# Optimization experiments

Measured on AMD Instinct MI355X. Metric: run time of the kernel, lower is better.

Reference implementation:

```python
import jax, jax.numpy as jnp
import numpy as np

M, S = 1024, 256   # keyframe intervals x IMU steps per interval
K = M + 1          # keyframes

# ---- quaternion utils (xyzw convention, as pypose) ----

def quat_mul(q, r):
    qx, qy, qz, qw = q[..., 0], q[..., 1], q[..., 2], q[..., 3]
    rx, ry, rz, rw = r[..., 0], r[..., 1], r[..., 2], r[..., 3]
    return jnp.stack([
        qw * rx + qx * rw + qy * rz - qz * ry,
        qw * ry - qx * rz + qy * rw + qz * rx,
        qw * rz + qx * ry - qy * rx + qz * rw,
        qw * rw - qx * rx - qy * ry - qz * rz], axis=-1)

def quat_conj(q):
    return jnp.concatenate([-q[..., :3], q[..., 3:4]], axis=-1)

def quat_exp(phi):
    theta = jnp.linalg.norm(phi, axis=-1, keepdims=True)
    half = 0.5 * theta
    small = theta < 1e-6
    k = jnp.where(small, 0.5 - theta * theta / 48.0,
                  jnp.sin(half) / jnp.where(small, 1.0, theta))
    return jnp.concatenate([phi * k, jnp.cos(half)], axis=-1)

def quat_log(q):
    v, w = q[..., :3], q[..., 3:4]
    n = jnp.linalg.norm(v, axis=-1, keepdims=True)
    small = n < 1e-6
    theta = 2.0 * jnp.arctan2(n, w)
    scale = jnp.where(small, 2.0 / jnp.where(jnp.abs(w) < 1e-6, 1.0, w),
                      theta / jnp.where(small, 1.0, n))
    return v * scale

def quat_to_mat(q):
    x, y, z, w = q[..., 0], q[..., 1], q[..., 2], q[..., 3]
    r = jnp.stack([
        1 - 2 * (y * y + z * z), 2 * (x * y - z * w), 2 * (x * z + y * w),
        2 * (x * y + z * w), 1 - 2 * (x * x + z * z), 2 * (y * z - x * w),
        2 * (x * z - y * w), 2 * (y * z + x * w), 1 - 2 * (x * x + y * y)], axis=-1)
    return r.reshape(q.shape[:-1] + (3, 3))

def skew(v):
    x, y, z = v[..., 0], v[..., 1], v[..., 2]
    o = jnp.zeros_like(x)
    return jnp.stack([o, -z, y, z, o, -x, -y, x, o], axis=-1).reshape(v.shape[:-1] + (3, 3))

def build_F(R, a, w):
    # batched 15x15 continuous-time state-transition matrix (F_t in source)
    m = R.shape[0]
    I3 = jnp.eye(3, dtype=R.dtype)
    F = jnp.zeros((m, 15, 15), R.dtype)
    F = F.at[:, 0:3, 3:6].set(I3)
    F = F.at[:, 3:6, 6:9].set(-jnp.einsum('mij,mjk->mik', R, skew(a)))
    F = F.at[:, 3:6, 9:12].set(-R)
    F = F.at[:, 6:9, 6:9].set(-skew(w))
    F = F.at[:, 6:9, 12:15].set(-I3)
    return F

def imu_loss(acc, gyro, dt, bias_a, bias_w, g, init_rot, init_pos, init_vel,
             gt_rot, gt_pos, gt_vel, weights=(1.0, 1.0, 1.0)):
    m, s, _ = acc.shape
    dtype = acc.dtype
    I15 = jnp.eye(15, dtype=dtype)
    q0 = jnp.broadcast_to(jnp.array([0., 0., 0., 1.], dtype), (m, 4))
    carry0 = (q0, jnp.zeros((m, 3), dtype), jnp.zeros((m, 3), dtype),
              jnp.broadcast_to(I15, (m, 15, 15)))
    xs = (jnp.swapaxes(dt, 0, 1), jnp.swapaxes(acc, 0, 1), jnp.swapaxes(gyro, 0, 1),
          jnp.swapaxes(bias_a, 0, 1), jnp.swapaxes(bias_w, 0, 1))

    def step(carry, x):
        q, v, p, J = carry
        dti, a, w, ba, bw = x
        d = dti[:, None]
        a_w = jnp.einsum('mij,mj->mi', quat_to_mat(q), a)   # accel in segment-start frame
        p = p + v * d + 0.5 * a_w * d * d
        v = v + a_w * d
        q = quat_mul(q, quat_exp(w * d))
        R = quat_to_mat(q)                                  # post-update rotation (F_t usage)
        F = build_F(R, a - ba, w - bw)
        J = jnp.einsum('mij,mjk->mik', I15 + dti[:, None, None] * F, J)
        return (q, v, p, J), None

    (gamma_hat, beta_hat, alpha_hat, Jac), _ = jax.lax.scan(step, carry0, xs)

    ba0, bw0 = bias_a[:, 0, :], bias_w[:, 0, :]   # bias at keyframe start (kf index)
    alpha = (alpha_hat + jnp.einsum('mij,mj->mi', Jac[:, 0:3, 9:12], ba0)
             + jnp.einsum('mij,mj->mi', Jac[:, 0:3, 12:15], bw0))
    beta = (beta_hat + jnp.einsum('mij,mj->mi', Jac[:, 3:6, 9:12], ba0)
            + jnp.einsum('mij,mj->mi', Jac[:, 3:6, 12:15], bw0))
    dtheta = 0.5 * jnp.einsum('mij,mj->mi', Jac[:, 6:9, 12:15], bw0)
    gamma = quat_mul(gamma_hat, jnp.concatenate([dtheta, jnp.ones((m, 1), dtype)], axis=-1))

    def rot_step(r, dq):
        r2 = quat_mul(r, dq)
        return r2, r2
    _, rots = jax.lax.scan(rot_step, init_rot, gamma)
    rot = jnp.concatenate([init_rot[None], rots], axis=0)   # [K,4]

    kf_dt = jnp.sum(dt, axis=1)[:, None]                    # [M,1]
    R_wb = quat_to_mat(rot[:m])
    dvel = -g[None, :] * kf_dt + jnp.einsum('mij,mj->mi', R_wb, beta)
    vel = jnp.cumsum(jnp.concatenate([init_vel[None], dvel], axis=0), axis=0)
    dpos = (vel[:m] * kf_dt - 0.5 * g[None, :] * kf_dt * kf_dt
            + jnp.einsum('mij,mj->mi', R_wb, alpha))
    pos = jnp.cumsum(jnp.concatenate([init_pos[None], dpos], axis=0), axis=0)

    rot_err = quat_log(quat_mul(quat_conj(gt_rot), rot))
    return jnp.concatenate([weights[0] * rot_err,
                            weights[1] * (gt_pos - pos) ** 2,
                            weights[2] * (gt_vel - vel) ** 2], axis=0)  # [3K,3]

def setup_inputs() -> dict:
    key = jax.random.key(0)
    ks = jax.random.split(key, 11)
    f32 = jnp.float32
    def unit_quat(k, shape):
        q = jax.random.normal(k, shape + (4,), f32)
        return q / jnp.linalg.norm(q, axis=-1, keepdims=True)
    return {
        'acc': jax.random.normal(ks[0], (M, S, 3), f32),
        'gyro': 0.1 * jax.random.normal(ks[1], (M, S, 3), f32),
        'dt': 0.005 * jax.random.uniform(ks[2], (M, S), f32),  # ~200Hz IMU
        'bias_a': 0.01 * jax.random.normal(ks[3], (M, S, 3), f32),
        'bias_w': 0.01 * jax.random.normal(ks[4], (M, S, 3), f32),
        'g': jnp.array([0.0, 0.0, 9.81007], f32),
        'init_rot': unit_quat(ks[5], ()),
        'init_pos': jax.random.normal(ks[6], (3,), f32),
        'init_vel': jax.random.normal(ks[7], (3,), f32),
        'gt_rot': unit_quat(ks[8], (K,)),
        'gt_pos': jax.random.normal(ks[9], (K, 3), f32),
        'gt_vel': jax.random.normal(ks[10], (K, 3), f32),
    }

def reference(acc, gyro, dt, bias_a, bias_w, g, init_rot, init_pos, init_vel,
              gt_rot, gt_pos, gt_vel):
    return imu_loss(acc, gyro, dt, bias_a, bias_w, g, init_rot, init_pos, init_vel,
                    gt_rot, gt_pos, gt_vel)
```

## Files before the change

### kernel.cpp

```cpp
#include <hip/hip_runtime.h>
#include <math.h>

#define NM 1024
#define NS 256
#define NK 1025
#define CS 4
#define NC 64

struct Q4 { float x, y, z, w; };

__device__ __forceinline__ Q4 qmul(const Q4 a, const Q4 b) {
    Q4 o;
    o.x = a.w*b.x + a.x*b.w + a.y*b.z - a.z*b.y;
    o.y = a.w*b.y - a.x*b.z + a.y*b.w + a.z*b.x;
    o.z = a.w*b.z + a.x*b.y - a.y*b.x + a.z*b.w;
    o.w = a.w*b.w - a.x*b.x - a.y*b.y - a.z*b.z;
    return o;
}

__device__ __forceinline__ void q2m(const Q4 q, float* R) {
    float x = q.x, y = q.y, z = q.z, w = q.w;
    R[0] = 1.f - 2.f*(y*y + z*z); R[1] = 2.f*(x*y - z*w);       R[2] = 2.f*(x*z + y*w);
    R[3] = 2.f*(x*y + z*w);       R[4] = 1.f - 2.f*(x*x + z*z); R[5] = 2.f*(y*z - x*w);
    R[6] = 2.f*(x*z - y*w);       R[7] = 2.f*(y*z + x*w);       R[8] = 1.f - 2.f*(x*x + y*y);
}

__device__ __forceinline__ void m3mul(float* o, const float* X, const float* Y) {
    #pragma unroll
    for (int r = 0; r < 3; ++r)
        #pragma unroll
        for (int c = 0; c < 3; ++c)
            o[r*3+c] = X[r*3+0]*Y[c] + X[r*3+1]*Y[3+c] + X[r*3+2]*Y[6+c];
}

__device__ __forceinline__ void m3v(float* o, const float* X, const float* v) {
    o[0] = X[0]*v[0] + X[1]*v[1] + X[2]*v[2];
    o[1] = X[3]*v[0] + X[4]*v[1] + X[5]*v[2];
    o[2] = X[6]*v[0] + X[7]*v[1] + X[8]*v[2];
}

__device__ __forceinline__ void skmul(float* o, float x, float y, float z, const float* M) {
    #pragma unroll
    for (int c = 0; c < 3; ++c) {
        float m0 = M[c], m1 = M[3+c], m2 = M[6+c];
        o[c]   = -z*m1 + y*m2;
        o[3+c] =  z*m0 - x*m2;
        o[6+c] = -y*m0 + x*m1;
    }
}

__device__ __forceinline__ void crossv(float* o, float x, float y, float z, const float* v) {
    o[0] = -z*v[1] + y*v[2];
    o[1] =  z*v[0] - x*v[2];
    o[2] = -y*v[0] + x*v[1];
}

__device__ __forceinline__ void ld12(float* dst, const float4* src) {
    float4 t0 = src[0], t1 = src[1], t2 = src[2];
    dst[0]=t0.x; dst[1]=t0.y; dst[2] =t0.z; dst[3] =t0.w;
    dst[4]=t1.x; dst[5]=t1.y; dst[6] =t1.z; dst[7] =t1.w;
    dst[8]=t2.x; dst[9]=t2.y; dst[10]=t2.z; dst[11]=t2.w;
}

__global__ __launch_bounds__(256, 2) void imu_phase1(
    const float* __restrict__ acc, const float* __restrict__ gyro,
    const float* __restrict__ dt, const float* __restrict__ bias_a,
    const float* __restrict__ bias_w, float* __restrict__ ws)
{
    const int lane = threadIdx.x & 63;
    const int m    = blockIdx.x * 4 + (threadIdx.x >> 6);
    const int c    = lane;

    float av[12], gv[12], bav[12], bwv[12], dtv[4];
    ld12(av,  (const float4*)(acc    + (size_t)m*NS*3) + c*3);
    ld12(gv,  (const float4*)(gyro   + (size_t)m*NS*3) + c*3);
    ld12(bav, (const float4*)(bias_a + (size_t)m*NS*3) + c*3);
    ld12(bwv, (const float4*)(bias_w + (size_t)m*NS*3) + c*3);
    {
        float4 t = ((const float4*)(dt + (size_t)m*NS))[c];
        dtv[0]=t.x; dtv[1]=t.y; dtv[2]=t.z; dtv[3]=t.w;
    }

    float ba0[3], bw0[3];
    ba0[0] = __shfl(bav[0], 0, 64); ba0[1] = __shfl(bav[1], 0, 64); ba0[2] = __shfl(bav[2], 0, 64);
    bw0[0] = __shfl(bwv[0], 0, 64); bw0[1] = __shfl(bwv[1], 0, 64); bw0[2] = __shfl(bwv[2], 0, 64);

    Q4 fq = {0.f, 0.f, 0.f, 1.f};
    float G[9] = {1.f,0.f,0.f, 0.f,1.f,0.f, 0.f,0.f,1.f};
    float T = 0.f;
    float u[3] = {0.f}, z[3] = {0.f};
    float A[9]  = {1.f,0.f,0.f, 0.f,1.f,0.f, 0.f,0.f,1.f};
    float Bmv[3] = {0.f};
    float M1v[3] = {0.f}, N[9] = {0.f}, nnv[3] = {0.f};
    float K1v[3] = {0.f}, K2a[9] = {0.f}, k2bv[3] = {0.f};

    #pragma unroll
    for (int j = 0; j < CS; ++j) {
        float d  = dtv[j];
        float ax = av[j*3+0], ay = av[j*3+1], az = av[j*3+2];
        float gx = gv[j*3+0], gy = gv[j*3+1], gz = gv[j*3+2];
        float abx = ax - bav[j*3+0], aby = ay - bav[j*3+1], abz = az - bav[j*3+2];
        float wbx = gx - bwv[j*3+0], wby = gy - bwv[j*3+1], wbz = gz - bwv[j*3+2];

        #pragma unroll
        for (int i = 0; i < 3; ++i) { K1v[i] += d*M1v[i]; k2bv[i] += d*nnv[i]; }
        #pragma unroll
        for (int i = 0; i < 9; ++i) K2a[i] += d*N[i];

        float ga0 = G[0]*ax + G[1]*ay + G[2]*az;
        float ga1 = G[3]*ax + G[4]*ay + G[5]*az;
        float ga2 = G[6]*ax + G[7]*ay + G[8]*az;
        float hd2 = 0.5f*d*d;
        z[0] += d*u[0] + hd2*ga0;
        z[1] += d*u[1] + hd2*ga1;
        z[2] += d*u[2] + hd2*ga2;
        u[0] += d*ga0; u[1] += d*ga1; u[2] += d*ga2;
        T += d;

        float phx = gx*d, phy = gy*d, phz = gz*d;
        float th2 = phx*phx + phy*phy + phz*phz;
        float k  = 0.5f - th2*(1.0f/48.0f);
        float ew = 1.0f - th2*0.125f;
        Q4 e = {phx*k, phy*k, phz*k, ew};
        fq = qmul(fq, e);
        q2m(fq, G);

        {
            float gb[3]; m3v(gb, G, ba0);
            M1v[0] += d*gb[0]; M1v[1] += d*gb[1]; M1v[2] += d*gb[2];
        }
        {
            float SA[9], GX[9];
            skmul(SA, abx, aby, abz, A);
            m3mul(GX, G, SA);
            #pragma unroll
            for (int i = 0; i < 9; ++i) N[i] += d*GX[i];
        }
        {
            float cb[3], gc[3];
            crossv(cb, abx, aby, abz, Bmv);
            m3v(gc, G, cb);
            nnv[0] += d*gc[0]; nnv[1] += d*gc[1]; nnv[2] += d*gc[2];
        }
        {
            float WA[9];
            skmul(WA, wbx, wby, wbz, A);
            #pragma unroll
            for (int i = 0; i < 9; ++i) A[i] -= d*WA[i];
        }
        {
            float cw[3];
            crossv(cw, wbx, wby, wbz, Bmv);
            Bmv[0] -= d*(cw[0] + bw0[0]);
            Bmv[1] -= d*(cw[1] + bw0[1]);
            Bmv[2] -= d*(cw[2] + bw0[2]);
        }
    }

    Q4 qi = fq;
    #pragma unroll
    for (int off = 1; off < 64; off <<= 1) {
        Q4 y;
        y.x = __shfl_up(qi.x, off, 64);
        y.y = __shfl_up(qi.y, off, 64);
        y.z = __shfl_up(qi.z, off, 64);
        y.w = __shfl_up(qi.w, off, 64);
        if (lane >= off) qi = qmul(y, qi);
    }
    Q4 qf;
    qf.x = __shfl(qi.x, 63, 64);
    qf.y = __shfl(qi.y, 63, 64);
    qf.z = __shfl(qi.z, 63, 64);
    qf.w = __shfl(qi.w, 63, 64);
    Q4 qp;
    qp.x = __shfl_up(qi.x, 1, 64);
    qp.y = __shfl_up(qi.y, 1, 64);
    qp.z = __shfl_up(qi.z, 1, 64);
    qp.w = __shfl_up(qi.w, 1, 64);
    if (lane == 0) { qp.x = 0.f; qp.y = 0.f; qp.z = 0.f; qp.w = 1.f; }
    float R[9]; q2m(qp, R);

    float bvec[3] = {Bmv[0], Bmv[1], Bmv[2]};
    #pragma unroll
    for (int off = 1; off < 64; off <<= 1) {
        float yA[9], yb[3];
        #pragma unroll
        for (int i = 0; i < 9; ++i) yA[i] = __shfl_up(A[i], off, 64);
        yb[0] = __shfl_up(bvec[0], off, 64);
        yb[1] = __shfl_up(bvec[1], off, 64);
        yb[2] = __shfl_up(bvec[2], off, 64);
        if (lane >= off) {
            float nA[9], nb[3];
            m3mul(nA, A, yA);
            m3v(nb, A, yb);
            #pragma unroll
            for (int i = 0; i < 9; ++i) A[i] = nA[i];
            bvec[0] = nb[0] + bvec[0];
            bvec[1] = nb[1] + bvec[1];
            bvec[2] = nb[2] + bvec[2];
        }
    }
    float Q2fv[3];
    Q2fv[0] = __shfl(bvec[0], 63, 64);
    Q2fv[1] = __shfl(bvec[1], 63, 64);
    Q2fv[2] = __shfl(bvec[2], 63, 64);
    float qv[3];
    qv[0] = __shfl_up(bvec[0], 1, 64);
    qv[1] = __shfl_up(bvec[1], 1, 64);
    qv[2] = __shfl_up(bvec[2], 1, 64);
    if (lane == 0) { qv[0] = 0.f; qv[1] = 0.f; qv[2] = 0.f; }

    float S = T;
    #pragma unroll
    for (int off = 1; off < 64; off <<= 1) {
        float y = __shfl_down(S, off, 64);
        if (lane + off < 64) S += y;
    }
    float Tsuf = S - T;

    float nq[3], kq[3];
    m3v(nq, N, qv);
    m3v(kq, K2a, qv);
    float t1[3] = { u[0] - M1v[0] - nq[0] - nnv[0],
                    u[1] - M1v[1] - nq[1] - nnv[1],
                    u[2] - M1v[2] - nq[2] - nnv[2] };
    float t2[3] = { z[0] - K1v[0] - kq[0] - k2bv[0],
                    z[1] - K1v[1] - kq[1] - k2bv[1],
                    z[2] - K1v[2] - kq[2] - k2bv[2] };
    float bc[3], ac[3];
    m3v(bc, R, t1);
    m3v(ac, R, t2);
    ac[0] += Tsuf*bc[0]; ac[1] += Tsuf*bc[1]; ac[2] += Tsuf*bc[2];

    #pragma unroll
    for (int off = 1; off < 64; off <<= 1) {
        #pragma unroll
        for (int i = 0; i < 3; ++i) {
            bc[i] += __shfl_xor(bc[i], off, 64);
            ac[i] += __shfl_xor(ac[i], off, 64);
        }
    }

    if (lane != 0) return;

    float dthx = 0.5f*Q2fv[0], dthy = 0.5f*Q2fv[1], dthz = 0.5f*Q2fv[2];
    Q4 dq = {dthx, dthy, dthz, 1.0f};
    Q4 gamma = qmul(qf, dq);

    float* g_gamma = ws;
    float* g_beta  = ws + 4*NM;
    float* g_alpha = ws + 7*NM;
    float* g_kf    = ws + 10*NM;
    g_gamma[m*4+0] = gamma.x; g_gamma[m*4+1] = gamma.y;
    g_gamma[m*4+2] = gamma.z; g_gamma[m*4+3] = gamma.w;
    g_beta[m*3+0] = bc[0];  g_beta[m*3+1] = bc[1];  g_beta[m*3+2] = bc[2];
    g_alpha[m*3+0] = ac[0]; g_alpha[m*3+1] = ac[1]; g_alpha[m*3+2] = ac[2];
    g_kf[m] = S;
}

__global__ __launch_bounds__(1024) void imu_phase2(
    const float* __restrict__ ws, const float* __restrict__ g,
    const float* __restrict__ init_rot, const float* __restrict__ init_pos,
    const float* __restrict__ init_vel, const float* __restrict__ gt_rot,
    const float* __restrict__ gt_pos, const float* __restrict__ gt_vel,
    float* __restrict__ out)
{
    __shared__ float4 srot[NK];
    __shared__ float  svel[NK][3];
    __shared__ float  spos[NK][3];
    __shared__ float4 qtot[16];
    __shared__ float  vtot[16][3];
    __shared__ float  ptot[16][3];

    const int tid  = threadIdx.x;
    const int lane = tid & 63;
    const int w    = tid >> 6;

    const float* g_gamma = ws;
    const float* g_beta  = ws + 4*NM;
    const float* g_alpha = ws + 7*NM;
    const float* g_kf    = ws + 10*NM;

    Q4 qinit = {init_rot[0], init_rot[1], init_rot[2], init_rot[3]};

    Q4 q = {g_gamma[tid*4+0], g_gamma[tid*4+1], g_gamma[tid*4+2], g_gamma[tid*4+3]};
    #pragma unroll
    for (int off = 1; off < 64; off <<= 1) {
        Q4 y;
        y.x = __shfl_up(q.x, off, 64);
        y.y = __shfl_up(q.y, off, 64);
        y.z = __shfl_up(q.z, off, 64);
        y.w = __shfl_up(q.w, off, 64);
        if (lane >= off) q = qmul(y, q);
    }
    if (lane == 63) qtot[w] = make_float4(q.x, q.y, q.z, q.w);
    __syncthreads();
    {
        Q4 pre = {0.f, 0.f, 0.f, 1.f};
        for (int j = 0; j < w; ++j) {
            float4 tq = qtot[j];
            pre = qmul(pre, Q4{tq.x, tq.y, tq.z, tq.w});
        }
        q = qmul(pre, q);
    }
    Q4 rot = qmul(qinit, q);
    srot[tid+1] = make_float4(rot.x, rot.y, rot.z, rot.w);
    if (tid == 0) srot[0] = make_float4(qinit.x, qinit.y, qinit.z, qinit.w);
    __syncthreads();

    const float gx = g[0], gy = g[1], gz = g[2];
    const float iv0 = init_vel[0], iv1 = init_vel[1], iv2 = init_vel[2];
    const float ip0 = init_pos[0], ip1 = init_pos[1], ip2 = init_pos[2];

    float4 r4 = srot[tid];
    Q4 rq = {r4.x, r4.y, r4.z, r4.w};
    float Rw[9]; q2m(rq, Rw);
    float kf = g_kf[tid];
    float bx = g_beta[tid*3+0], by = g_beta[tid*3+1], bz = g_beta[tid*3+2];
    float axm = g_alpha[tid*3+0], aym = g_alpha[tid*3+1], azm = g_alpha[tid*3+2];

    float dv0 = -gx*kf + Rw[0]*bx + Rw[1]*by + Rw[2]*bz;
    float dv1 = -gy*kf + Rw[3]*bx + Rw[4]*by + Rw[5]*bz;
    float dv2 = -gz*kf + Rw[6]*bx + Rw[7]*by + Rw[8]*bz;
    float s0 = dv0, s1 = dv1, s2 = dv2;
    #pragma unroll
    for (int off = 1; off < 64; off <<= 1) {
        float y0 = __shfl_up(s0, off, 64);
        float y1 = __shfl_up(s1, off, 64);
        float y2 = __shfl_up(s2, off, 64);
        if (lane >= off) { s0 += y0; s1 += y1; s2 += y2; }
    }
    if (lane == 63) { vtot[w][0] = s0; vtot[w][1] = s1; vtot[w][2] = s2; }
    __syncthreads();
    {
        float p0 = 0.f, p1 = 0.f, p2 = 0.f;
        for (int j = 0; j < w; ++j) { p0 += vtot[j][0]; p1 += vtot[j][1]; p2 += vtot[j][2]; }
        s0 += p0; s1 += p1; s2 += p2;
    }
    svel[tid+1][0] = iv0 + s0; svel[tid+1][1] = iv1 + s1; svel[tid+1][2] = iv2 + s2;
    if (tid == 0) { svel[0][0] = iv0; svel[0][1] = iv1; svel[0][2] = iv2; }

    float vm0 = iv0 + s0 - dv0, vm1 = iv1 + s1 - dv1, vm2 = iv2 + s2 - dv2;

    float dp0 = vm0*kf - 0.5f*gx*kf*kf + Rw[0]*axm + Rw[1]*aym + Rw[2]*azm;
    float dp1 = vm1*kf - 0.5f*gy*kf*kf + Rw[3]*axm + Rw[4]*aym + Rw[5]*azm;
    float dp2 = vm2*kf - 0.5f*gz*kf*kf + Rw[6]*axm + Rw[7]*aym + Rw[8]*azm;
    float t0 = dp0, t1 = dp1, t2 = dp2;
    #pragma unroll
    for (int off = 1; off < 64; off <<= 1) {
        float y0 = __shfl_up(t0, off, 64);
        float y1 = __shfl_up(t1, off, 64);
        float y2 = __shfl_up(t2, off, 64);
        if (lane >= off) { t0 += y0; t1 += y1; t2 += y2; }
    }
    if (lane == 63) { ptot[w][0] = t0; ptot[w][1] = t1; ptot[w][2] = t2; }
    __syncthreads();
    {
        float p0 = 0.f, p1 = 0.f, p2 = 0.f;
        for (int j = 0; j < w; ++j) { p0 += ptot[j][0]; p1 += ptot[j][1]; p2 += ptot[j][2]; }
        t0 += p0; t1 += p1; t2 += p2;
    }
    spos[tid+1][0] = ip0 + t0; spos[tid+1][1] = ip1 + t1; spos[tid+1][2] = ip2 + t2;
    if (tid == 0) { spos[0][0] = ip0; spos[0][1] = ip1; spos[0][2] = ip2; }
    __syncthreads();

    for (int k = tid; k < NK; k += 1024) {
        float4 rr = srot[k];
        Q4 rk = {rr.x, rr.y, rr.z, rr.w};
        Q4 gc = {-gt_rot[k*4+0], -gt_rot[k*4+1], -gt_rot[k*4+2], gt_rot[k*4+3]};
        Q4 e = qmul(gc, rk);
        float n2 = e.x*e.x + e.y*e.y + e.z*e.z;
        float n = sqrtf(n2);
        float theta = 2.f*atan2f(n, e.w);
        float scale;
        if (n < 1e-6f) {
            float wd = (fabsf(e.w) < 1e-6f) ? 1.f : e.w;
            scale = 2.f/wd;
        } else {
            scale = theta/n;
        }
        out[k*3+0] = e.x*scale;
        out[k*3+1] = e.y*scale;
        out[k*3+2] = e.z*scale;

        float d0 = gt_pos[k*3+0] - spos[k][0];
        float d1 = gt_pos[k*3+1] - spos[k][1];
        float d2 = gt_pos[k*3+2] - spos[k][2];
        out[(NK+k)*3+0] = d0*d0;
        out[(NK+k)*3+1] = d1*d1;
        out[(NK+k)*3+2] = d2*d2;

        float e0 = gt_vel[k*3+0] - svel[k][0];
        float e1 = gt_vel[k*3+1] - svel[k][1];
        float e2 = gt_vel[k*3+2] - svel[k][2];
        out[(2*NK+k)*3+0] = e0*e0;
        out[(2*NK+k)*3+1] = e1*e1;
        out[(2*NK+k)*3+2] = e2*e2;
    }
}

extern "C" void kernel_launch(void* const* d_in, const int* in_sizes, int n_in,
                              void* d_out, int out_size, void* d_ws, size_t ws_size,
                              hipStream_t stream) {
    const float* acc      = (const float*)d_in[0];
    const float* gyro     = (const float*)d_in[1];
    const float* dt       = (const float*)d_in[2];
    const float* bias_a   = (const float*)d_in[3];
    const float* bias_w   = (const float*)d_in[4];
    const float* g        = (const float*)d_in[5];
    const float* init_rot = (const float*)d_in[6];
    const float* init_pos = (const float*)d_in[7];
    const float* init_vel = (const float*)d_in[8];
    const float* gt_rot   = (const float*)d_in[9];
    const float* gt_pos   = (const float*)d_in[10];
    const float* gt_vel   = (const float*)d_in[11];
    float* ws  = (float*)d_ws;
    float* out = (float*)d_out;

    imu_phase1<<<NM/4, 256, 0, stream>>>(acc, gyro, dt, bias_a, bias_w, ws);
    imu_phase2<<<1, 1024, 0, stream>>>(ws, g, init_rot, init_pos, init_vel,
                                       gt_rot, gt_pos, gt_vel, out);
}
```

Before: 20.45 us.

## Assign one IMU step per thread with block-level cross-wave scan

Phase 1 moves from one wave per keyframe interval, with each lane integrating 4 steps serially, to one 256-thread block per interval with one step per thread. Each thread computes its own local rotation, transition and contribution terms. Wave-level scans are then stitched across the 4 waves through shared memory, and a final thread combines the per-wave results. The aim is to remove the serial per-lane recurrence and increase parallelism, at the cost of 4x more blocks, non-vectorised scalar loads, two block barriers and a serial tail in one thread.

```diff
diff --git a/kernel.cpp b/kernel.cpp
--- a/kernel.cpp
+++ b/kernel.cpp
@@ -4,8 +4,7 @@
 #define NM 1024
 #define NS 256
 #define NK 1025
-#define CS 4
-#define NC 64
+#define WPS 4
 
 struct Q4 { float x, y, z, w; };
 
@@ -39,125 +38,65 @@
     o[2] = X[6]*v[0] + X[7]*v[1] + X[8]*v[2];
 }
 
-__device__ __forceinline__ void skmul(float* o, float x, float y, float z, const float* M) {
-    #pragma unroll
-    for (int c = 0; c < 3; ++c) {
-        float m0 = M[c], m1 = M[3+c], m2 = M[6+c];
-        o[c]   = -z*m1 + y*m2;
-        o[3+c] =  z*m0 - x*m2;
-        o[6+c] = -y*m0 + x*m1;
-    }
-}
-
-__device__ __forceinline__ void crossv(float* o, float x, float y, float z, const float* v) {
-    o[0] = -z*v[1] + y*v[2];
-    o[1] =  z*v[0] - x*v[2];
-    o[2] = -y*v[0] + x*v[1];
-}
-
-__device__ __forceinline__ void ld12(float* dst, const float4* src) {
-    float4 t0 = src[0], t1 = src[1], t2 = src[2];
-    dst[0]=t0.x; dst[1]=t0.y; dst[2] =t0.z; dst[3] =t0.w;
-    dst[4]=t1.x; dst[5]=t1.y; dst[6] =t1.z; dst[7] =t1.w;
-    dst[8]=t2.x; dst[9]=t2.y; dst[10]=t2.z; dst[11]=t2.w;
-}
-
-__global__ __launch_bounds__(256, 2) void imu_phase1(
+__global__ __launch_bounds__(256, 4) void imu_phase1(
     const float* __restrict__ acc, const float* __restrict__ gyro,
     const float* __restrict__ dt, const float* __restrict__ bias_a,
     const float* __restrict__ bias_w, float* __restrict__ ws)
 {
-    const int lane = threadIdx.x & 63;
-    const int m    = blockIdx.x * 4 + (threadIdx.x >> 6);
-    const int c    = lane;
-
-    float av[12], gv[12], bav[12], bwv[12], dtv[4];
-    ld12(av,  (const float4*)(acc    + (size_t)m*NS*3) + c*3);
-    ld12(gv,  (const float4*)(gyro   + (size_t)m*NS*3) + c*3);
-    ld12(bav, (const float4*)(bias_a + (size_t)m*NS*3) + c*3);
-    ld12(bwv, (const float4*)(bias_w + (size_t)m*NS*3) + c*3);
-    {
-        float4 t = ((const float4*)(dt + (size_t)m*NS))[c];
-        dtv[0]=t.x; dtv[1]=t.y; dtv[2]=t.z; dtv[3]=t.w;
-    }
-
-    float ba0[3], bw0[3];
-    ba0[0] = __shfl(bav[0], 0, 64); ba0[1] = __shfl(bav[1], 0, 64); ba0[2] = __shfl(bav[2], 0, 64);
-    bw0[0] = __shfl(bwv[0], 0, 64); bw0[1] = __shfl(bwv[1], 0, 64); bw0[2] = __shfl(bwv[2], 0, 64);
-
-    Q4 fq = {0.f, 0.f, 0.f, 1.f};
-    float G[9] = {1.f,0.f,0.f, 0.f,1.f,0.f, 0.f,0.f,1.f};
-    float T = 0.f;
-    float u[3] = {0.f}, z[3] = {0.f};
-    float A[9]  = {1.f,0.f,0.f, 0.f,1.f,0.f, 0.f,0.f,1.f};
-    float Bmv[3] = {0.f};
-    float M1v[3] = {0.f}, N[9] = {0.f}, nnv[3] = {0.f};
-    float K1v[3] = {0.f}, K2a[9] = {0.f}, k2bv[3] = {0.f};
-
-    #pragma unroll
-    for (int j = 0; j < CS; ++j) {
-        float d  = dtv[j];
-        float ax = av[j*3+0], ay = av[j*3+1], az = av[j*3+2];
-        float gx = gv[j*3+0], gy = gv[j*3+1], gz = gv[j*3+2];
-        float abx = ax - bav[j*3+0], aby = ay - bav[j*3+1], abz = az - bav[j*3+2];
-        float wbx = gx - bwv[j*3+0], wby = gy - bwv[j*3+1], wbz = gz - bwv[j*3+2];
-
-        #pragma unroll
-        for (int i = 0; i < 3; ++i) { K1v[i] += d*M1v[i]; k2bv[i] += d*nnv[i]; }
-        #pragma unroll
-        for (int i = 0; i < 9; ++i) K2a[i] += d*N[i];
-
-        float ga0 = G[0]*ax + G[1]*ay + G[2]*az;
-        float ga1 = G[3]*ax + G[4]*ay + G[5]*az;
-        float ga2 = G[6]*ax + G[7]*ay + G[8]*az;
-        float hd2 = 0.5f*d*d;
-        z[0] += d*u[0] + hd2*ga0;
-        z[1] += d*u[1] + hd2*ga1;
-        z[2] += d*u[2] + hd2*ga2;
-        u[0] += d*ga0; u[1] += d*ga1; u[2] += d*ga2;
-        T += d;
-
-        float phx = gx*d, phy = gy*d, phz = gz*d;
-        float th2 = phx*phx + phy*phy + phz*phz;
-        float k  = 0.5f - th2*(1.0f/48.0f);
-        float ew = 1.0f - th2*0.125f;
-        Q4 e = {phx*k, phy*k, phz*k, ew};
-        fq = qmul(fq, e);
-        q2m(fq, G);
-
-        {
-            float gb[3]; m3v(gb, G, ba0);
-            M1v[0] += d*gb[0]; M1v[1] += d*gb[1]; M1v[2] += d*gb[2];
-        }
-        {
-            float SA[9], GX[9];
-            skmul(SA, abx, aby, abz, A);
-            m3mul(GX, G, SA);
-            #pragma unroll
-            for (int i = 0; i < 9; ++i) N[i] += d*GX[i];
-        }
-        {
-            float cb[3], gc[3];
-            crossv(cb, abx, aby, abz, Bmv);
-            m3v(gc, G, cb);
-            nnv[0] += d*gc[0]; nnv[1] += d*gc[1]; nnv[2] += d*gc[2];
-        }
-        {
-            float WA[9];
-            skmul(WA, wbx, wby, wbz, A);
-            #pragma unroll
-            for (int i = 0; i < 9; ++i) A[i] -= d*WA[i];
-        }
-        {
-            float cw[3];
-            crossv(cw, wbx, wby, wbz, Bmv);
-            Bmv[0] -= d*(cw[0] + bw0[0]);
-            Bmv[1] -= d*(cw[1] + bw0[1]);
-            Bmv[2] -= d*(cw[2] + bw0[2]);
-        }
-    }
-
-    Q4 qi = fq;
+    __shared__ float sE[WPS][4];
+    __shared__ float sA[WPS][9];
+    __shared__ float sb[WPS][3];
+    __shared__ float sT[WPS];
+    __shared__ float sBC[WPS][3];
+    __shared__ float sAC[WPS][3];
+
+    const int tid  = threadIdx.x;
+    const int w    = tid >> 6;
+    const int lane = tid & 63;
+    const int m    = blockIdx.x;
+    const int s    = tid;
+
+    const size_t b3 = (size_t)m * NS * 3;
+
+    float d  = dt[(size_t)m * NS + s];
+    float a0 = acc[b3 + s*3+0], a1 = acc[b3 + s*3+1], a2 = acc[b3 + s*3+2];
+    float g0 = gyro[b3 + s*3+0], g1 = gyro[b3 + s*3+1], g2 = gyro[b3 + s*3+2];
+    float bas0 = bias_a[b3 + s*3+0], bas1 = bias_a[b3 + s*3+1], bas2 = bias_a[b3 + s*3+2];
+    float bws0 = bias_w[b3 + s*3+0], bws1 = bias_w[b3 + s*3+1], bws2 = bias_w[b3 + s*3+2];
+    float ba0x = bias_a[b3+0], ba0y = bias_a[b3+1], ba0z = bias_a[b3+2];
+    float bw0x = bias_w[b3+0], bw0y = bias_w[b3+1], bw0z = bias_w[b3+2];
+
+    float abx = a0 - bas0, aby = a1 - bas1, abz = a2 - bas2;
+    float wbx = g0 - bws0, wby = g1 - bws1, wbz = g2 - bws2;
+
+    float phx = g0*d, phy = g1*d, phz = g2*d;
+    float th2 = phx*phx + phy*phy + phz*phz;
+    float kq  = 0.5f - th2*(1.0f/48.0f);
+    float ew  = 1.0f - th2*0.125f;
+    Q4 E = {phx*kq, phy*kq, phz*kq, ew};
+    float G[9]; q2m(E, G);
+
+    float u0 = d*a0, u1 = d*a1, u2 = d*a2;
+    float hd2 = 0.5f*d*d;
+    float z0 = hd2*a0, z1 = hd2*a1, z2 = hd2*a2;
+
+    float M1v[3];
+    M1v[0] = d*(G[0]*ba0x + G[1]*ba0y + G[2]*ba0z);
+    M1v[1] = d*(G[3]*ba0x + G[4]*ba0y + G[5]*ba0z);
+    M1v[2] = d*(G[6]*ba0x + G[7]*ba0y + G[8]*ba0z);
+
+    float N[9];
+    N[0] = d*( G[1]*abz - G[2]*aby); N[3] = d*( G[4]*abz - G[5]*aby); N[6] = d*( G[7]*abz - G[8]*aby);
+    N[1] = d*(-G[0]*abz + G[2]*abx); N[4] = d*(-G[3]*abz + G[5]*abx); N[7] = d*(-G[6]*abz + G[8]*abx);
+    N[2] = d*( G[0]*aby - G[1]*abx); N[5] = d*( G[3]*aby - G[4]*abx); N[8] = d*( G[6]*aby - G[7]*abx);
+
+    float A[9];
+    A[0] = 1.f;      A[1] =  d*wbz;  A[2] = -d*wby;
+    A[3] = -d*wbz;   A[4] = 1.f;     A[5] =  d*wbx;
+    A[6] =  d*wby;   A[7] = -d*wbx;  A[8] = 1.f;
+    float bvec[3] = {-d*bw0x, -d*bw0y, -d*bw0z};
+
+    Q4 qi = E; float Ti = d;
     #pragma unroll
     for (int off = 1; off < 64; off <<= 1) {
         Q4 y;
@@ -165,22 +104,19 @@
         y.y = __shfl_up(qi.y, off, 64);
         y.z = __shfl_up(qi.z, off, 64);
         y.w = __shfl_up(qi.w, off, 64);
-        if (lane >= off) qi = qmul(y, qi);
-    }
-    Q4 qf;
-    qf.x = __shfl(qi.x, 63, 64);
-    qf.y = __shfl(qi.y, 63, 64);
-    qf.z = __shfl(qi.z, 63, 64);
-    qf.w = __shfl(qi.w, 63, 64);
+        float yT = __shfl_up(Ti, off, 64);
+        if (lane >= off) { qi = qmul(y, qi); Ti += yT; }
+    }
+    float Tw = __shfl(Ti, 63, 64);
+    float Tsuf = Tw - Ti;
     Q4 qp;
     qp.x = __shfl_up(qi.x, 1, 64);
     qp.y = __shfl_up(qi.y, 1, 64);
     qp.z = __shfl_up(qi.z, 1, 64);
     qp.w = __shfl_up(qi.w, 1, 64);
     if (lane == 0) { qp.x = 0.f; qp.y = 0.f; qp.z = 0.f; qp.w = 1.f; }
-    float R[9]; q2m(qp, R);
-
-    float bvec[3] = {Bmv[0], Bmv[1], Bmv[2]};
+    float Rloc[9]; q2m(qp, Rloc);
+
     #pragma unroll
     for (int off = 1; off < 64; off <<= 1) {
         float yA[9], yb[3];
@@ -200,36 +136,49 @@
             bvec[2] = nb[2] + bvec[2];
         }
     }
-    float Q2fv[3];
-    Q2fv[0] = __shfl(bvec[0], 63, 64);
-    Q2fv[1] = __shfl(bvec[1], 63, 64);
-    Q2fv[2] = __shfl(bvec[2], 63, 64);
-    float qv[3];
-    qv[0] = __shfl_up(bvec[0], 1, 64);
-    qv[1] = __shfl_up(bvec[1], 1, 64);
-    qv[2] = __shfl_up(bvec[2], 1, 64);
-    if (lane == 0) { qv[0] = 0.f; qv[1] = 0.f; qv[2] = 0.f; }
-
-    float S = T;
-    #pragma unroll
-    for (int off = 1; off < 64; off <<= 1) {
-        float y = __shfl_down(S, off, 64);
-        if (lane + off < 64) S += y;
-    }
-    float Tsuf = S - T;
-
-    float nq[3], kq[3];
-    m3v(nq, N, qv);
-    m3v(kq, K2a, qv);
-    float t1[3] = { u[0] - M1v[0] - nq[0] - nnv[0],
-                    u[1] - M1v[1] - nq[1] - nnv[1],
-                    u[2] - M1v[2] - nq[2] - nnv[2] };
-    float t2[3] = { z[0] - K1v[0] - kq[0] - k2bv[0],
-                    z[1] - K1v[1] - kq[1] - k2bv[1],
-                    z[2] - K1v[2] - kq[2] - k2bv[2] };
+    float qvloc[3], Aexc[9];
+    qvloc[0] = __shfl_up(bvec[0], 1, 64);
+    qvloc[1] = __shfl_up(bvec[1], 1, 64);
+    qvloc[2] = __shfl_up(bvec[2], 1, 64);
+    #pragma unroll
+    for (int i = 0; i < 9; ++i) Aexc[i] = __shfl_up(A[i], 1, 64);
+    if (lane == 0) {
+        qvloc[0] = qvloc[1] = qvloc[2] = 0.f;
+        Aexc[0] = 1.f; Aexc[1] = 0.f; Aexc[2] = 0.f;
+        Aexc[3] = 0.f; Aexc[4] = 1.f; Aexc[5] = 0.f;
+        Aexc[6] = 0.f; Aexc[7] = 0.f; Aexc[8] = 1.f;
+    }
+
+    if (lane == 63) {
+        sE[w][0] = qi.x; sE[w][1] = qi.y; sE[w][2] = qi.z; sE[w][3] = qi.w;
+        #pragma unroll
+        for (int i = 0; i < 9; ++i) sA[w][i] = A[i];
+        sb[w][0] = bvec[0]; sb[w][1] = bvec[1]; sb[w][2] = bvec[2];
+        sT[w] = Ti;
+    }
+    __syncthreads();
+
+    float bprev[3] = {0.f, 0.f, 0.f};
+    for (int j = 0; j < w; ++j) {
+        float t[3]; m3v(t, sA[j], bprev);
+        bprev[0] = t[0] + sb[j][0];
+        bprev[1] = t[1] + sb[j][1];
+        bprev[2] = t[2] + sb[j][2];
+    }
+    float TsufW = 0.f;
+    for (int j = w+1; j < WPS; ++j) TsufW += sT[j];
+
+    float qv[3]; m3v(qv, Aexc, bprev);
+    qv[0] += qvloc[0]; qv[1] += qvloc[1]; qv[2] += qvloc[2];
+
+    float nq[3]; m3v(nq, N, qv);
+    float t1[3] = { u0 - M1v[0] - nq[0],
+                    u1 - M1v[1] - nq[1],
+                    u2 - M1v[2] - nq[2] };
+    float t2[3] = { z0, z1, z2 };
     float bc[3], ac[3];
-    m3v(bc, R, t1);
-    m3v(ac, R, t2);
+    m3v(bc, Rloc, t1);
+    m3v(ac, Rloc, t2);
     ac[0] += Tsuf*bc[0]; ac[1] += Tsuf*bc[1]; ac[2] += Tsuf*bc[2];
 
     #pragma unroll
@@ -241,21 +190,59 @@
         }
     }
 
-    if (lane != 0) return;
-
-    float dthx = 0.5f*Q2fv[0], dthy = 0.5f*Q2fv[1], dthz = 0.5f*Q2fv[2];
-    Q4 dq = {dthx, dthy, dthz, 1.0f};
-    Q4 gamma = qmul(qf, dq);
-
-    float* g_gamma = ws;
-    float* g_beta  = ws + 4*NM;
-    float* g_alpha = ws + 7*NM;
-    float* g_kf    = ws + 10*NM;
-    g_gamma[m*4+0] = gamma.x; g_gamma[m*4+1] = gamma.y;
-    g_gamma[m*4+2] = gamma.z; g_gamma[m*4+3] = gamma.w;
-    g_beta[m*3+0] = bc[0];  g_beta[m*3+1] = bc[1];  g_beta[m*3+2] = bc[2];
-    g_alpha[m*3+0] = ac[0]; g_alpha[m*3+1] = ac[1]; g_alpha[m*3+2] = ac[2];
-    g_kf[m] = S;
+    if (lane == 0) {
+        Q4 qpre = {0.f, 0.f, 0.f, 1.f};
+        for (int j = 0; j < w; ++j) {
+            Q4 ej = {sE[j][0], sE[j][1], sE[j][2], sE[j][3]};
+            qpre = qmul(qpre, ej);
+        }
+        float Rpre[9]; q2m(qpre, Rpre);
+        float t[3] = { ac[0] + TsufW*bc[0], ac[1] + TsufW*bc[1], ac[2] + TsufW*bc[2] };
+        float bcp[3], acp[3];
+        m3v(bcp, Rpre, bc);
+        m3v(acp, Rpre, t);
+        sBC[w][0] = bcp[0]; sBC[w][1] = bcp[1]; sBC[w][2] = bcp[2];
+        sAC[w][0] = acp[0]; sAC[w][1] = acp[1]; sAC[w][2] = acp[2];
+    }
+    __syncthreads();
+
+    if (tid == 0) {
+        float beta[3]  = {0.f, 0.f, 0.f};
+        float alpha[3] = {0.f, 0.f, 0.f};
+        float kf = 0.f;
+        #pragma unroll
+        for (int j = 0; j < WPS; ++j) {
+            beta[0]  += sBC[j][0]; beta[1]  += sBC[j][1]; beta[2]  += sBC[j][2];
+            alpha[0] += sAC[j][0]; alpha[1] += sAC[j][1]; alpha[2] += sAC[j][2];
+            kf += sT[j];
+        }
+        Q4 qf = {sE[0][0], sE[0][1], sE[0][2], sE[0][3]};
+        #pragma unroll
+        for (int j = 1; j < WPS; ++j) {
+            Q4 ej = {sE[j][0], sE[j][1], sE[j][2], sE[j][3]};
+            qf = qmul(qf, ej);
+        }
+        float bfin[3] = {0.f, 0.f, 0.f};
+        #pragma unroll
+        for (int j = 0; j < WPS; ++j) {
+            float t[3]; m3v(t, sA[j], bfin);
+            bfin[0] = t[0] + sb[j][0];
+            bfin[1] = t[1] + sb[j][1];
+            bfin[2] = t[2] + sb[j][2];
+        }
+        Q4 dq = {0.5f*bfin[0], 0.5f*bfin[1], 0.5f*bfin[2], 1.0f};
+        Q4 gamma = qmul(qf, dq);
+
+        float* g_gamma = ws;
+        float* g_beta  = ws + 4*NM;
+        float* g_alpha = ws + 7*NM;
+        float* g_kf    = ws + 10*NM;
+        g_gamma[m*4+0] = gamma.x; g_gamma[m*4+1] = gamma.y;
+        g_gamma[m*4+2] = gamma.z; g_gamma[m*4+3] = gamma.w;
+        g_beta[m*3+0] = beta[0];  g_beta[m*3+1] = beta[1];  g_beta[m*3+2] = beta[2];
+        g_alpha[m*3+0] = alpha[0]; g_alpha[m*3+1] = alpha[1]; g_alpha[m*3+2] = alpha[2];
+        g_kf[m] = kf;
+    }
 }
 
 __global__ __launch_bounds__(1024) void imu_phase2(
@@ -417,7 +404,7 @@
     float* ws  = (float*)d_ws;
     float* out = (float*)d_out;
 
-    imu_phase1<<<NM/4, 256, 0, stream>>>(acc, gyro, dt, bias_a, bias_w, ws);
+    imu_phase1<<<NM, 256, 0, stream>>>(acc, gyro, dt, bias_a, bias_w, ws);
     imu_phase2<<<1, 1024, 0, stream>>>(ws, g, init_rot, init_pos, init_vel,
                                        gt_rot, gt_pos, gt_vel, out);
 }
```

Result: slower. 26.41 us (+29.1%).
